# Optimization experiments

Measured on AMD Instinct MI355X. Metric: run time of the kernel, lower is better.

The kernel has to match this reference:

```python
import jax, jax.numpy as jnp
import numpy as np

# Circuit geometry (matches QNN(sequence_length=16384, quantum_layer_quantity=4, output_quantity=64, entangler='basic'))
SEQ_LEN = 16384
N_ADDR = 14                      # ceil(log2(16384))
N_DATA = 4                       # UNIQUE_NUCLEOTIDE_QUANTITY
N_WIRES = N_ADDR + N_DATA        # 18
DIM = 2 ** N_WIRES               # 262144
N_LAYERS = 4
OUT = 64
BATCH = 32


def _apply_rx(state, theta, w):
    """Apply RX(theta) on wire w (wire 0 = most significant bit)."""
    c = jnp.cos(theta / 2).astype(jnp.complex64)
    s = (-1j * jnp.sin(theta / 2)).astype(jnp.complex64)
    U = jnp.stack([jnp.stack([c, s]), jnp.stack([s, c])])  # [2,2]
    B = state.shape[0]
    st = state.reshape(B, 2 ** w, 2, -1)
    st = jnp.einsum('ij,bajc->baic', U, st)
    return st.reshape(B, DIM)


def _apply_cnot(state, c, t):
    """CNOT with control wire c, target wire t."""
    B = state.shape[0]
    st = state.reshape((B,) + (2,) * N_WIRES)
    c_ax, t_ax = 1 + c, 1 + t
    p0 = jnp.take(st, 0, axis=c_ax)
    p1 = jnp.take(st, 1, axis=c_ax)
    t_ax_r = t_ax - 1 if t_ax > c_ax else t_ax
    p1 = jnp.flip(p1, axis=t_ax_r)  # X on target within control=1 block
    st = jnp.stack([p0, p1], axis=c_ax)
    return st.reshape(B, DIM)


def _circuit_probs(x, qweights):
    # Encoding: address register stays |0...0>, so among all multi-controlled
    # BasisEmbeddings only index 0 (control pattern all zeros) applies its X
    # gates. Resulting basis state index = bits of x[:,0,:] on the 4 data
    # wires (least-significant bits), address bits = 0.
    bits = x[:, 0, :]  # [B, 4]
    pw = jnp.asarray([8, 4, 2, 1], dtype=jnp.int32)
    idx = jnp.sum(bits * pw, axis=-1)  # [B]
    state = jax.nn.one_hot(idx, DIM, dtype=jnp.complex64)  # [B, DIM]
    # BasicEntanglerLayers: per layer, RX on every wire then a CNOT ring.
    for l in range(N_LAYERS):
        for w in range(N_WIRES):
            state = _apply_rx(state, qweights[l, w], w)
        for w in range(N_WIRES):
            state = _apply_cnot(state, w, (w + 1) % N_WIRES)
    return jnp.abs(state) ** 2  # qml.probs over all wires -> [B, DIM] float32


def setup_inputs() -> dict:
    key = jax.random.key(0)
    kx, kw, kW = jax.random.split(key, 3)
    x = jax.random.randint(kx, (BATCH, SEQ_LEN, N_DATA), 0, 2, dtype=jnp.int32)
    qweights = jax.random.uniform(kw, (N_LAYERS, N_WIRES), dtype=jnp.float32,
                                  maxval=2.0 * np.pi)
    W = jax.random.normal(kW, (OUT, DIM), dtype=jnp.float32) / np.sqrt(DIM)
    b = jnp.zeros((OUT,), dtype=jnp.float32)
    return {"x": x, "qweights": qweights, "W": W, "b": b}


def reference(x, qweights, W, b):
    probs = _circuit_probs(x, qweights)          # [B, 2^18]
    logits = probs @ W.T + b                     # [B, 64]
    return jax.nn.sigmoid(logits)
```

## Files before the change

kernel.cpp:

```cpp
#include <hip/hip_runtime.h>
#include <math.h>


#define DIM (1 << 18)
#define NW 18
#define CH 128
#define CPB 4
#define NMM (DIM / (CH * CPB))

#define PAD16(i) ((i) + ((i) >> 4))

typedef short short8 __attribute__((ext_vector_type(8)));
typedef float f32x4  __attribute__((ext_vector_type(4)));

__device__ __forceinline__ unsigned perm18(unsigned i) {
    unsigned s = i;
    s ^= s >> 1; s ^= s >> 2; s ^= s >> 4; s ^= s >> 8; s ^= s >> 16;
    unsigned out = s & 0x1FFFFu;
    out |= ((s ^ (i >> 17)) & 1u) << 17;
    return out;
}

__device__ __forceinline__ unsigned pinv18(unsigned b) {
    unsigned t = b & 0x1FFFFu;
    unsigned u = (t ^ (t >> 1)) & 0xFFFFu;
    unsigned i17 = ((b >> 17) ^ t) & 1u;
    unsigned i16 = ((t >> 16) ^ i17) & 1u;
    return u | (i16 << 16) | (i17 << 17);
}

__device__ __forceinline__ unsigned ginv9(unsigned x) {
    x ^= x >> 1; x ^= x >> 2; x ^= x >> 4; x ^= x >> 8;
    return x & 511u;
}

__device__ __forceinline__ void bfly(float2& a0, float2& a1, float c, float s) {
    float2 n0 = make_float2(c * a0.x + s * a1.y, c * a0.y - s * a1.x);
    float2 n1 = make_float2(c * a1.x + s * a0.y, c * a1.y - s * a0.x);
    a0 = n0; a1 = n1;
}

__device__ __forceinline__ short f2bf(float x) {
    unsigned u = __float_as_uint(x);
    return (short)((u + 0x7FFFu + ((u >> 16) & 1u)) >> 16);
}

template<int RB>
__device__ __forceinline__ void slotRound(float2* t, int m, float2 g0, float2 g1) {
    constexpr int B = 1 << RB;
    int low = m & (B - 1);
    int high = m >> RB;
    int ib = (high << (RB + 2)) | low;
    int p00 = PAD16(ib), p01 = PAD16(ib | B), p10 = PAD16(ib | 2 * B), p11 = PAD16(ib | 3 * B);
    float2 e00 = t[p00], e01 = t[p01], e10 = t[p10], e11 = t[p11];
    bfly(e00, e01, g0.x, g0.y);
    bfly(e10, e11, g0.x, g0.y);
    bfly(e00, e10, g1.x, g1.y);
    bfly(e01, e11, g1.x, g1.y);
    t[p00] = e00; t[p01] = e01; t[p10] = e10; t[p11] = e11;
}

__device__ __forceinline__ void kaTail(float2* t, int tid, const float2* gsh,
                                       float2* __restrict__ out, unsigned B9) {
    slotRound<1>(t, tid, gsh[1], gsh[2]); __syncthreads();
    slotRound<3>(t, tid, gsh[3], gsh[4]); __syncthreads();
    slotRound<5>(t, tid, gsh[5], gsh[6]); __syncthreads();
    int low = tid & 127, high = tid >> 7;
    int ib = (high << 9) | low;
    float2 a0 = t[PAD16(ib)], a1 = t[PAD16(ib | 128)];
    float2 a2 = t[PAD16(ib | 256)], a3 = t[PAD16(ib | 384)];
    bfly(a0, a1, gsh[7].x, gsh[7].y);
    bfly(a2, a3, gsh[7].x, gsh[7].y);
    bfly(a0, a2, gsh[8].x, gsh[8].y);
    bfly(a1, a3, gsh[8].x, gsh[8].y);
    unsigned ob = ((unsigned)high << 17) | (B9 << 9) | (unsigned)low;
    out[ob] = a0; out[ob + 128] = a1; out[ob + 256] = a2; out[ob + 384] = a3;
}

__global__ __launch_bounds__(256) void kInit(float2* __restrict__ out, const float* qw) {
    __shared__ float2 t[1088];
    __shared__ float2 gsh[10];
    int tid = threadIdx.x;
    if (tid < 10) {
        int p = (tid == 9) ? 17 : tid;
        float th = qw[1 * NW + (17 - p)] * 0.5f;
        gsh[tid] = make_float2(cosf(th), sinf(th));
    }
    float c[NW], s[NW];
#pragma unroll
    for (int w = 0; w < NW; ++w) {
        float th = qw[w] * 0.5f;
        c[w] = cosf(th); s[w] = sinf(th);
    }
    unsigned B9 = blockIdx.x;
    float2 e[2][2];
#pragma unroll
    for (int p17 = 0; p17 < 2; ++p17)
#pragma unroll
        for (int b0 = 0; b0 < 2; ++b0) {
            unsigned b = ((unsigned)p17 << 17) | (B9 << 9) | ((unsigned)tid << 1) | (unsigned)b0;
            unsigned i = pinv18(b);
            float m = 1.0f;
#pragma unroll
            for (int p = 0; p < 18; ++p)
                m *= ((i >> p) & 1u) ? s[17 - p] : c[17 - p];
            int k4 = __popc(i) & 3;
            if      (k4 == 0) e[p17][b0] = make_float2( m, 0.f);
            else if (k4 == 1) e[p17][b0] = make_float2(0.f, -m);
            else if (k4 == 2) e[p17][b0] = make_float2(-m, 0.f);
            else              e[p17][b0] = make_float2(0.f,  m);
        }
    __syncthreads();
    bfly(e[0][0], e[0][1], gsh[0].x, gsh[0].y);
    bfly(e[1][0], e[1][1], gsh[0].x, gsh[0].y);
    bfly(e[0][0], e[1][0], gsh[9].x, gsh[9].y);
    bfly(e[0][1], e[1][1], gsh[9].x, gsh[9].y);
    int sb = tid << 1;
    t[PAD16(sb)] = e[0][0];       t[PAD16(sb | 1)] = e[0][1];
    t[PAD16(sb | 512)] = e[1][0]; t[PAD16(sb | 513)] = e[1][1];
    __syncthreads();
    kaTail(t, tid, gsh, out, B9);
}

__global__ __launch_bounds__(256) void kA(const float2* __restrict__ in,
                                          float2* __restrict__ out,
                                          const float* qw, int layer) {
    __shared__ float2 t[1088];
    __shared__ float2 gsh[10];
    int tid = threadIdx.x;
    if (tid < 10) {
        int p = (tid == 9) ? 17 : tid;
        float th = qw[layer * NW + (17 - p)] * 0.5f;
        gsh[tid] = make_float2(cosf(th), sinf(th));
    }
    unsigned B9 = blockIdx.x;
    unsigned C = pinv18(B9 << 9);
    unsigned c9 = C & 511u;
    unsigned base0 = C & ~511u;
    unsigned base1 = base0 ^ 0x30000u;
    float2 v[2][2];
#pragma unroll
    for (int ee = 0; ee < 2; ++ee)
#pragma unroll
        for (int r = 0; r < 2; ++r)
            v[ee][r] = in[(ee ? base1 : base0) + (unsigned)tid + 256u * r];
#pragma unroll
    for (int ee = 0; ee < 2; ++ee)
#pragma unroll
        for (int r = 0; r < 2; ++r) {
            unsigned k = (unsigned)tid + 256u * r;
            unsigned x = (k ^ c9) & 511u;
            unsigned bl = ginv9(x);
            unsigned p17 = ((unsigned)__popc(x) ^ (unsigned)ee) & 1u;
            t[PAD16((p17 << 9) | bl)] = v[ee][r];
        }
    __syncthreads();
    {
        int s00 = tid << 1;
        int p00 = PAD16(s00), p01 = PAD16(s00 | 1), p10 = PAD16(s00 | 512), p11 = PAD16(s00 | 513);
        float2 e00 = t[p00], e01 = t[p01], e10 = t[p10], e11 = t[p11];
        bfly(e00, e01, gsh[0].x, gsh[0].y);
        bfly(e10, e11, gsh[0].x, gsh[0].y);
        bfly(e00, e10, gsh[9].x, gsh[9].y);
        bfly(e01, e11, gsh[9].x, gsh[9].y);
        t[p00] = e00; t[p01] = e01; t[p10] = e10; t[p11] = e11;
    }
    __syncthreads();
    kaTail(t, tid, gsh, out, B9);
}

__global__ __launch_bounds__(256) void kBC(float2* __restrict__ buf, float* probs,
                                           const float* qw, int layer) {
    __shared__ float2 t[1088];
    __shared__ float2 gsh[8];
    int tid = threadIdx.x;
    if (tid < 8) {
        float th = qw[layer * NW + (8 - tid)] * 0.5f;
        gsh[tid] = make_float2(cosf(th), sinf(th));
    }
    unsigned blk = blockIdx.x;
    unsigned ibase = ((blk >> 7) << 17) | ((blk & 127u) << 2) | 0u;
    int mh = tid >> 2, lo = tid & 3;
    ibase |= (unsigned)lo;
    float2 e0 = buf[((unsigned)(4 * mh + 0) << 9) | ibase];
    float2 e1 = buf[((unsigned)(4 * mh + 1) << 9) | ibase];
    float2 e2 = buf[((unsigned)(4 * mh + 2) << 9) | ibase];
    float2 e3 = buf[((unsigned)(4 * mh + 3) << 9) | ibase];
    __syncthreads();
    bfly(e0, e1, gsh[0].x, gsh[0].y);
    bfly(e2, e3, gsh[0].x, gsh[0].y);
    bfly(e0, e2, gsh[1].x, gsh[1].y);
    bfly(e1, e3, gsh[1].x, gsh[1].y);
    {
        int k = 4 * (4 * mh) + lo;
        t[PAD16(k)] = e0; t[PAD16(k + 4)] = e1; t[PAD16(k + 8)] = e2; t[PAD16(k + 12)] = e3;
    }
    __syncthreads();
    {
        int hb = ((mh >> 2) << 4) | (mh & 3);
        int p00 = PAD16(4 * hb + lo), p01 = PAD16(4 * (hb | 4) + lo);
        int p10 = PAD16(4 * (hb | 8) + lo), p11 = PAD16(4 * (hb | 12) + lo);
        float2 a0 = t[p00], a1 = t[p01], a2 = t[p10], a3 = t[p11];
        bfly(a0, a1, gsh[2].x, gsh[2].y);
        bfly(a2, a3, gsh[2].x, gsh[2].y);
        bfly(a0, a2, gsh[3].x, gsh[3].y);
        bfly(a1, a3, gsh[3].x, gsh[3].y);
        t[p00] = a0; t[p01] = a1; t[p10] = a2; t[p11] = a3;
    }
    __syncthreads();
    {
        int hb = ((mh >> 4) << 6) | (mh & 15);
        int p00 = PAD16(4 * hb + lo), p01 = PAD16(4 * (hb | 16) + lo);
        int p10 = PAD16(4 * (hb | 32) + lo), p11 = PAD16(4 * (hb | 48) + lo);
        float2 a0 = t[p00], a1 = t[p01], a2 = t[p10], a3 = t[p11];
        bfly(a0, a1, gsh[4].x, gsh[4].y);
        bfly(a2, a3, gsh[4].x, gsh[4].y);
        bfly(a0, a2, gsh[5].x, gsh[5].y);
        bfly(a1, a3, gsh[5].x, gsh[5].y);
        t[p00] = a0; t[p01] = a1; t[p10] = a2; t[p11] = a3;
    }
    __syncthreads();
    {
        int k = 4 * mh + lo;
        float2 a0 = t[PAD16(k)], a1 = t[PAD16(k + 256)], a2 = t[PAD16(k + 512)], a3 = t[PAD16(k + 768)];
        bfly(a0, a1, gsh[6].x, gsh[6].y);
        bfly(a2, a3, gsh[6].x, gsh[6].y);
        bfly(a0, a2, gsh[7].x, gsh[7].y);
        bfly(a1, a3, gsh[7].x, gsh[7].y);
        unsigned i0 = ((unsigned)(mh +   0) << 9) | ibase;
        unsigned i1 = ((unsigned)(mh +  64) << 9) | ibase;
        unsigned i2 = ((unsigned)(mh + 128) << 9) | ibase;
        unsigned i3 = ((unsigned)(mh + 192) << 9) | ibase;
        if (probs) {
            probs[perm18(i0)] = a0.x * a0.x + a0.y * a0.y;
            probs[perm18(i1)] = a1.x * a1.x + a1.y * a1.y;
            probs[perm18(i2)] = a2.x * a2.x + a2.y * a2.y;
            probs[perm18(i3)] = a3.x * a3.x + a3.y * a3.y;
        } else {
            buf[i0] = a0; buf[i1] = a1; buf[i2] = a2; buf[i3] = a3;
        }
    }
}

__global__ __launch_bounds__(256) void k_mm(const float* __restrict__ p0,
                                            const float* __restrict__ W,
                                            float* __restrict__ partial) {
    __shared__ short Wl[64][136];
    __shared__ short Pl[16][136];
    __shared__ unsigned Tsh[16];
    int tid = threadIdx.x;
    if (tid < 16) {
        unsigned v = (unsigned)tid;
#pragma unroll
        for (int r = 0; r < 4; ++r) v = perm18(v);
        Tsh[tid] = v;
    }
    __syncthreads();

    unsigned d00 = (unsigned)blockIdx.x * (CH * CPB);
    int wrow = tid >> 5;
    int wcol = (tid & 31) * 4;
    int prow = tid >> 7;
    int pcol = tid & 127;
    unsigned Tp[8];
#pragma unroll
    for (int t = 0; t < 8; ++t) Tp[t] = Tsh[prow + 2 * t];

    int lane = tid & 63, wv = tid >> 6;
    int arow = lane & 15, kg = (lane >> 4) * 8;
    f32x4 acc = {0.f, 0.f, 0.f, 0.f};

    float4 wr[8];
    float  pr[8];

#pragma unroll
    for (int t = 0; t < 8; ++t)
        wr[t] = *(const float4*)&W[(size_t)(wrow + 8 * t) * DIM + d00 + wcol];
#pragma unroll
    for (int t = 0; t < 8; ++t)
        pr[t] = p0[(d00 ^ (Tp[t] & ~127u)) + pcol];
#pragma unroll
    for (int t = 0; t < 8; ++t) {
        short4 b = make_short4(f2bf(wr[t].x), f2bf(wr[t].y), f2bf(wr[t].z), f2bf(wr[t].w));
        *(short4*)&Wl[wrow + 8 * t][wcol] = b;
    }
#pragma unroll
    for (int t = 0; t < 8; ++t)
        Pl[prow + 2 * t][pcol ^ (Tp[t] & 127u)] = f2bf(pr[t]);
    __syncthreads();

    for (int cc = 0; cc < CPB; ++cc) {
        if (cc + 1 < CPB) {
            unsigned d1 = d00 + (unsigned)(cc + 1) * CH;
#pragma unroll
            for (int t = 0; t < 8; ++t)
                wr[t] = *(const float4*)&W[(size_t)(wrow + 8 * t) * DIM + d1 + wcol];
#pragma unroll
            for (int t = 0; t < 8; ++t)
                pr[t] = p0[(d1 ^ (Tp[t] & ~127u)) + pcol];
        }
#pragma unroll
        for (int kk = 0; kk < 4; ++kk) {
            short8 a = *(const short8*)&Pl[arow][kk * 32 + kg];
            short8 b = *(const short8*)&Wl[16 * wv + arow][kk * 32 + kg];
            acc = __builtin_amdgcn_mfma_f32_16x16x32_bf16(a, b, acc, 0, 0, 0);
        }
        __syncthreads();
        if (cc + 1 < CPB) {
#pragma unroll
            for (int t = 0; t < 8; ++t) {
                short4 b = make_short4(f2bf(wr[t].x), f2bf(wr[t].y), f2bf(wr[t].z), f2bf(wr[t].w));
                *(short4*)&Wl[wrow + 8 * t][wcol] = b;
            }
#pragma unroll
            for (int t = 0; t < 8; ++t)
                Pl[prow + 2 * t][pcol ^ (Tp[t] & 127u)] = f2bf(pr[t]);
            __syncthreads();
        }
    }

    float* dst = partial + (size_t)blockIdx.x * 1024;
#pragma unroll
    for (int r = 0; r < 4; ++r) {
        int jrow = (lane >> 4) * 4 + r;
        dst[jrow * 64 + 16 * wv + (lane & 15)] = acc[r];
    }
}

__global__ __launch_bounds__(256) void k_finalize(const float* __restrict__ partial,
                                                  const float* __restrict__ bias,
                                                  const int* __restrict__ x,
                                                  float* __restrict__ out) {
    int b = blockIdx.x;
    int tid = threadIdx.x;
    int ji = tid & 15, ci = tid >> 4;
    int jo = b * 16 + ji;
    float sum = 0.f;
#pragma unroll 8
    for (int c = ci; c < NMM; c += 16)
        sum += partial[(size_t)c * 1024 + jo];
    __shared__ float red[16][17];
    __shared__ float lg[16];
    __shared__ int sidx[32];
    red[ci][ji] = sum;
    if (tid < 32) {
        const int* xb = x + (size_t)tid * (16384 * 4);
        sidx[tid] = 8 * xb[0] + 4 * xb[1] + 2 * xb[2] + xb[3];
    }
    __syncthreads();
    if (ci == 0) {
        float s = 0.f;
#pragma unroll
        for (int k = 0; k < 16; ++k) s += red[k][ji];
        lg[ji] = s + bias[jo & 63];
    }
    __syncthreads();
    int myidx = b >> 2, o0 = (b & 3) * 16;
#pragma unroll
    for (int r = 0; r < 2; ++r) {
        int slot = tid + 256 * r;
        int bb = slot >> 4, k = slot & 15;
        if (sidx[bb] == myidx) {
            float z = lg[k];
            out[bb * 64 + o0 + k] = 1.f / (1.f + expf(-z));
        }
    }
}

extern "C" void kernel_launch(void* const* d_in, const int* in_sizes, int n_in,
                              void* d_out, int out_size, void* d_ws, size_t ws_size,
                              hipStream_t stream) {
    const int*   x    = (const int*)d_in[0];
    const float* qw   = (const float*)d_in[1];
    const float* W    = (const float*)d_in[2];
    const float* bias = (const float*)d_in[3];
    float* out = (float*)d_out;

    char* ws = (char*)d_ws;
    float2*   buf0    = (float2*)(ws + (1ull << 20));
    float2*   buf1    = (float2*)(ws + (4ull << 20));
    float*    probs   = (float*)(ws + (8ull << 20));
    float*    partial = (float*)(ws + (16ull << 20));

    kInit<<<256, 256, 0, stream>>>(buf0, qw);
    kBC  <<<256, 256, 0, stream>>>(buf0, nullptr, qw, 1);
    kA   <<<256, 256, 0, stream>>>(buf0, buf1, qw, 2);
    kBC  <<<256, 256, 0, stream>>>(buf1, nullptr, qw, 2);
    kA   <<<256, 256, 0, stream>>>(buf1, buf0, qw, 3);
    kBC  <<<256, 256, 0, stream>>>(buf0, probs, qw, 3);

    k_mm<<<NMM, 256, 0, stream>>>(probs, W, partial);
    k_finalize<<<64, 256, 0, stream>>>(partial, bias, x, out);
}
```

Measured before the change: 56.30 us.

## Fuse all circuit and matmul phases into one persistent kernel with grid barriers

Replaces eight separate kernel launches with a single persistent kernel of 256 blocks that runs each phase in sequence, separated by atomic-counter grid barriers in global memory. The matmul phase is changed to 8 chunks per block so it also runs on exactly 256 blocks. This removes per-launch overhead and the inter-kernel gaps. In exchange it adds spin-wait barrier cost, requires all 256 blocks to be co-resident, and adds a memset before each launch.

Measured after the change: 209.3 us. 272% more time.

```diff
diff --git a/kernel.cpp b/kernel.cpp
--- a/kernel.cpp
+++ b/kernel.cpp
@@ -5,8 +5,8 @@
 #define DIM (1 << 18)
 #define NW 18
 #define CH 128
-#define CPB 4
-#define NMM (DIM / (CH * CPB))
+#define CPB 8
+#define NMM 256
 
 #define PAD16(i) ((i) + ((i) >> 4))
 
@@ -43,6 +43,23 @@
 __device__ __forceinline__ short f2bf(float x) {
     unsigned u = __float_as_uint(x);
     return (short)((u + 0x7FFFu + ((u >> 16) & 1u)) >> 16);
+}
+
+__device__ __forceinline__ void gbar(unsigned* bar, int k) {
+    __syncthreads();
+    if (threadIdx.x == 0) {
+        unsigned old = __hip_atomic_fetch_add(bar + 2 + k, 1u,
+                                              __ATOMIC_ACQ_REL, __HIP_MEMORY_SCOPE_AGENT);
+        if (old == 255u) {
+            __hip_atomic_store(bar, (unsigned)(k + 1),
+                               __ATOMIC_RELEASE, __HIP_MEMORY_SCOPE_AGENT);
+        } else {
+            while (__hip_atomic_load(bar, __ATOMIC_ACQUIRE,
+                                     __HIP_MEMORY_SCOPE_AGENT) < (unsigned)(k + 1))
+                __builtin_amdgcn_s_sleep(1);
+        }
+    }
+    __syncthreads();
 }
 
 template<int RB>
@@ -77,9 +94,7 @@
     out[ob] = a0; out[ob + 128] = a1; out[ob + 256] = a2; out[ob + 384] = a3;
 }
 
-__global__ __launch_bounds__(256) void kInit(float2* __restrict__ out, const float* qw) {
-    __shared__ float2 t[1088];
-    __shared__ float2 gsh[10];
+__device__ void ph_init(float2* t, float2* gsh, float2* __restrict__ out, const float* qw) {
     int tid = threadIdx.x;
     if (tid < 10) {
         int p = (tid == 9) ? 17 : tid;
@@ -122,11 +137,8 @@
     kaTail(t, tid, gsh, out, B9);
 }
 
-__global__ __launch_bounds__(256) void kA(const float2* __restrict__ in,
-                                          float2* __restrict__ out,
-                                          const float* qw, int layer) {
-    __shared__ float2 t[1088];
-    __shared__ float2 gsh[10];
+__device__ void ph_a(float2* t, float2* gsh, const float2* __restrict__ in,
+                     float2* __restrict__ out, const float* qw, int layer) {
     int tid = threadIdx.x;
     if (tid < 10) {
         int p = (tid == 9) ? 17 : tid;
@@ -169,17 +181,15 @@
     kaTail(t, tid, gsh, out, B9);
 }
 
-__global__ __launch_bounds__(256) void kBC(float2* __restrict__ buf, float* probs,
-                                           const float* qw, int layer) {
-    __shared__ float2 t[1088];
-    __shared__ float2 gsh[8];
+__device__ void ph_bc(float2* t, float2* gsh, float2* __restrict__ buf, float* probs,
+                      const float* qw, int layer) {
     int tid = threadIdx.x;
     if (tid < 8) {
         float th = qw[layer * NW + (8 - tid)] * 0.5f;
         gsh[tid] = make_float2(cosf(th), sinf(th));
     }
     unsigned blk = blockIdx.x;
-    unsigned ibase = ((blk >> 7) << 17) | ((blk & 127u) << 2) | 0u;
+    unsigned ibase = ((blk >> 7) << 17) | ((blk & 127u) << 2);
     int mh = tid >> 2, lo = tid & 3;
     ibase |= (unsigned)lo;
     float2 e0 = buf[((unsigned)(4 * mh + 0) << 9) | ibase];
@@ -242,12 +252,11 @@
     }
 }
 
-__global__ __launch_bounds__(256) void k_mm(const float* __restrict__ p0,
-                                            const float* __restrict__ W,
-                                            float* __restrict__ partial) {
-    __shared__ short Wl[64][136];
-    __shared__ short Pl[16][136];
-    __shared__ unsigned Tsh[16];
+__device__ void ph_mm(char* ldsraw, const float* __restrict__ p0,
+                      const float* __restrict__ W, float* __restrict__ partial) {
+    short (*Wl)[136] = (short(*)[136])ldsraw;
+    short (*Pl)[136] = (short(*)[136])(ldsraw + 17408);
+    unsigned* Tsh    = (unsigned*)(ldsraw + 21760);
     int tid = threadIdx.x;
     if (tid < 16) {
         unsigned v = (unsigned)tid;
@@ -327,10 +336,12 @@
     }
 }
 
-__global__ __launch_bounds__(256) void k_finalize(const float* __restrict__ partial,
-                                                  const float* __restrict__ bias,
-                                                  const int* __restrict__ x,
-                                                  float* __restrict__ out) {
+__device__ void ph_fin(char* ldsraw, const float* __restrict__ partial,
+                       const float* __restrict__ bias, const int* __restrict__ x,
+                       float* __restrict__ out) {
+    float (*red)[17] = (float(*)[17])ldsraw;
+    float* lg        = (float*)(ldsraw + 1152);
+    int*   sidx      = (int*)(ldsraw + 1280);
     int b = blockIdx.x;
     int tid = threadIdx.x;
     int ji = tid & 15, ci = tid >> 4;
@@ -339,9 +350,6 @@
 #pragma unroll 8
     for (int c = ci; c < NMM; c += 16)
         sum += partial[(size_t)c * 1024 + jo];
-    __shared__ float red[16][17];
-    __shared__ float lg[16];
-    __shared__ int sidx[32];
     red[ci][ji] = sum;
     if (tid < 32) {
         const int* xb = x + (size_t)tid * (16384 * 4);
@@ -365,6 +373,35 @@
             out[bb * 64 + o0 + k] = 1.f / (1.f + expf(-z));
         }
     }
+}
+
+__global__ __launch_bounds__(256) void k_all(const float* __restrict__ qw,
+                                             const float* __restrict__ W,
+                                             const int* __restrict__ x,
+                                             const float* __restrict__ bias,
+                                             float2* buf0, float2* buf1,
+                                             float* probs, float* partial,
+                                             float* out, unsigned* bar) {
+    __shared__ __align__(16) char ldsraw[21888];
+    float2* t   = (float2*)ldsraw;
+    float2* gsh = (float2*)(ldsraw + 8704);
+
+    ph_init(t, gsh, buf0, qw);
+    gbar(bar, 0);
+    ph_bc(t, gsh, buf0, nullptr, qw, 1);
+    gbar(bar, 1);
+    ph_a(t, gsh, buf0, buf1, qw, 2);
+    gbar(bar, 2);
+    ph_bc(t, gsh, buf1, nullptr, qw, 2);
+    gbar(bar, 3);
+    ph_a(t, gsh, buf1, buf0, qw, 3);
+    gbar(bar, 4);
+    ph_bc(t, gsh, buf0, probs, qw, 3);
+    gbar(bar, 5);
+    ph_mm(ldsraw, probs, W, partial);
+    gbar(bar, 6);
+    if (blockIdx.x < 64)
+        ph_fin(ldsraw, partial, bias, x, out);
 }
 
 extern "C" void kernel_launch(void* const* d_in, const int* in_sizes, int n_in,
@@ -377,18 +414,12 @@
     float* out = (float*)d_out;
 
     char* ws = (char*)d_ws;
+    unsigned* bar     = (unsigned*)ws;
     float2*   buf0    = (float2*)(ws + (1ull << 20));
     float2*   buf1    = (float2*)(ws + (4ull << 20));
     float*    probs   = (float*)(ws + (8ull << 20));
     float*    partial = (float*)(ws + (16ull << 20));
 
-    kInit<<<256, 256, 0, stream>>>(buf0, qw);
-    kBC  <<<256, 256, 0, stream>>>(buf0, nullptr, qw, 1);
-    kA   <<<256, 256, 0, stream>>>(buf0, buf1, qw, 2);
-    kBC  <<<256, 256, 0, stream>>>(buf1, nullptr, qw, 2);
-    kA   <<<256, 256, 0, stream>>>(buf1, buf0, qw, 3);
-    kBC  <<<256, 256, 0, stream>>>(buf0, probs, qw, 3);
-
-    k_mm<<<NMM, 256, 0, stream>>>(probs, W, partial);
-    k_finalize<<<64, 256, 0, stream>>>(partial, bias, x, out);
-}
+    hipMemsetAsync(bar, 0, 256, stream);
+    k_all<<<256, 256, 0, stream>>>(qw, W, x, bias, buf0, buf1, probs, partial, out, bar);
+}
```
